# Optimization experiments

Hardware: AMD Instinct MI355X
Metric: run time of the kernel (lower is better)

## Reference

```python
import jax, jax.numpy as jnp
import numpy as np

DIM = 2048
HIDDEN = int(DIM * 2.6)  # 5324, matches int(dim*2.6) in torch
BATCH = 16384
EPS = 1e-12  # F.normalize default eps


def rmsnorm(x, g):
    # F.normalize(x, dim=-1) * dim**-0.5 * g
    n = jnp.linalg.norm(x, axis=-1, keepdims=True)
    return x / jnp.maximum(n, EPS) * (DIM ** -0.5) * g


def setup_inputs() -> dict:
    key = jax.random.key(0)
    ks = jax.random.split(key, 12)
    s = DIM ** -0.5
    return {
        "x": jax.random.normal(ks[0], (BATCH, DIM), jnp.float32),
        "state": jax.random.normal(ks[1], (BATCH, DIM), jnp.float32),
        "g1": jnp.ones((DIM,), jnp.float32),
        "g2": jnp.ones((DIM,), jnp.float32),
        "in_proj_w": jax.random.normal(ks[2], (3 * DIM, DIM), jnp.float32) * s,
        "in_proj_b": jnp.zeros((3 * DIM,), jnp.float32),
        "out_proj_w": jax.random.normal(ks[3], (DIM, DIM), jnp.float32) * s,
        "out_proj_b": jnp.zeros((DIM,), jnp.float32),
        "w1": jax.random.normal(ks[4], (HIDDEN, DIM), jnp.float32) * s,
        "w2": jax.random.normal(ks[5], (HIDDEN, DIM), jnp.float32) * s,
        "w3": jax.random.normal(ks[6], (DIM, HIDDEN), jnp.float32) * (HIDDEN ** -0.5),
    }


def reference(x, state, g1, g2, in_proj_w, in_proj_b, out_proj_w, out_proj_b, w1, w2, w3):
    h = x + state
    res = h
    hn = rmsnorm(h, g1)
    # MultiheadAttention with seq_len == 1: softmax over a single key is
    # exactly 1 for every head, so attn_out == out_proj(v_proj(hn)).
    wv = in_proj_w[2 * DIM:]
    bv = in_proj_b[2 * DIM:]
    v = hn @ wv.T + bv                      # [B, D]
    attn_out = v @ out_proj_w.T + out_proj_b
    h = res + attn_out
    hn2 = rmsnorm(h, g2)
    ffn = (jax.nn.silu(hn2 @ w1.T) * (hn2 @ w2.T)) @ w3.T
    return h + ffn
```

## Files before the change

### kernel.cpp

```cpp
#include <hip/hip_runtime.h>
#include <hip/hip_bf16.h>
#include <cstdint>
#include <cstddef>

#define DIMN   2048
#define BATCH  16384
#define HID    5324
#define HP     5376

typedef __bf16 bf16;
typedef __attribute__((ext_vector_type(8))) __bf16 bf16x8;
typedef __attribute__((ext_vector_type(4))) float floatx4;

#define GAS __attribute__((address_space(1)))
#define LAS __attribute__((address_space(3)))

__device__ __forceinline__ void async_copy16(const bf16* g, bf16* l) {
    __builtin_amdgcn_global_load_lds((const GAS uint32_t*)g, (LAS uint32_t*)l, 16, 0, 0);
}

template<int MODE>
__global__ __launch_bounds__(512, 2) void gemm_bt(
    const bf16* __restrict__ A, const bf16* __restrict__ W,
    const int K, const int N,
    const float* __restrict__ bias,
    float* __restrict__ f32io,
    bf16* __restrict__ bf16io)
{
    __shared__ __align__(16) bf16 lds[49152];

    const int tid  = threadIdx.x;
    const int lane = tid & 63;
    const int wv   = tid >> 6;
    const int wm   = wv >> 2;
    const int wn   = wv & 3;

    const int gx  = gridDim.x;
    const int nwg = gx * gridDim.y;
    int lin = blockIdx.y * gx + blockIdx.x;
    if ((nwg & 7) == 0) lin = (lin & 7) * (nwg >> 3) + (lin >> 3);
    const int bx = lin % gx, by = lin / gx;
    const int blockRow = by << 8;
    const int blockCol = bx << 8;

    const int sg = ((lane & 3) ^ ((lane >> 3) & 3)) * 8;
    const bf16* pA[2];
    const bf16* pB[2];
#pragma unroll
    for (int i = 0; i < 2; i++) {
        pA[i] = A + (size_t)(blockRow + i * 128 + wv * 16 + (lane >> 2)) * K + sg;
        pB[i] = W + (size_t)(blockCol + i * 128 + wv * 16 + (lane >> 2)) * K + sg;
    }

    const int m16 = lane & 15, quad = lane >> 4;
    const int rg = (quad ^ ((m16 >> 1) & 3)) * 8;
    const int aBase = (wm * 128 + m16) * 32 + rg;
    const int bBase = 8192 + (wn * 64 + m16) * 32 + rg;

    floatx4 acc[8][4];
    const floatx4 zero = {0.f, 0.f, 0.f, 0.f};
#pragma unroll
    for (int i = 0; i < 8; i++)
#pragma unroll
        for (int j = 0; j < 4; j++) acc[i][j] = zero;

    const int nt = K >> 5;

#pragma unroll
    for (int i = 0; i < 2; i++) {
        async_copy16(pA[i], &lds[i * 4096 + wv * 512]);
        async_copy16(pB[i], &lds[8192 + i * 4096 + wv * 512]);
    }
#pragma unroll
    for (int i = 0; i < 2; i++) { pA[i] += 32; pB[i] += 32; }
#pragma unroll
    for (int i = 0; i < 2; i++) {
        async_copy16(pA[i], &lds[16384 + i * 4096 + wv * 512]);
        async_copy16(pB[i], &lds[16384 + 8192 + i * 4096 + wv * 512]);
    }
#pragma unroll
    for (int i = 0; i < 2; i++) { pA[i] += 32; pB[i] += 32; }
    asm volatile("s_waitcnt vmcnt(4)" ::: "memory");
    __builtin_amdgcn_s_barrier();

    int sCur = 0, sNxt = 32768;
    for (int t = 0; t < nt; ++t) {
        const bool pf = (t + 2) < nt;

        if (pf) {
            async_copy16(pA[0], &lds[sNxt + wv * 512]);
            async_copy16(pA[1], &lds[sNxt + 4096 + wv * 512]);
        }
        bf16x8 bfr[4], afr[4];
#pragma unroll
        for (int j = 0; j < 4; j++) bfr[j] = *(const bf16x8*)&lds[sCur + bBase + j * 512];
#pragma unroll
        for (int i = 0; i < 4; i++) afr[i] = *(const bf16x8*)&lds[sCur + aBase + i * 512];
        __builtin_amdgcn_s_setprio(1);
#pragma unroll
        for (int i = 0; i < 4; i++)
#pragma unroll
            for (int j = 0; j < 4; j++)
                acc[i][j] = __builtin_amdgcn_mfma_f32_16x16x32_bf16(afr[i], bfr[j], acc[i][j], 0, 0, 0);
        __builtin_amdgcn_s_setprio(0);
        __builtin_amdgcn_s_barrier();

        if (pf) {
            async_copy16(pB[0], &lds[sNxt + 8192 + wv * 512]);
            async_copy16(pB[1], &lds[sNxt + 8192 + 4096 + wv * 512]);
            pA[0] += 32; pA[1] += 32; pB[0] += 32; pB[1] += 32;
        }
#pragma unroll
        for (int i = 0; i < 4; i++) afr[i] = *(const bf16x8*)&lds[sCur + aBase + 2048 + i * 512];
        __builtin_amdgcn_s_setprio(1);
#pragma unroll
        for (int i = 0; i < 4; i++)
#pragma unroll
            for (int j = 0; j < 4; j++)
                acc[i + 4][j] = __builtin_amdgcn_mfma_f32_16x16x32_bf16(afr[i], bfr[j], acc[i + 4][j], 0, 0, 0);
        __builtin_amdgcn_s_setprio(0);

        if (pf) { asm volatile("s_waitcnt vmcnt(4)" ::: "memory"); }
        else    { asm volatile("s_waitcnt vmcnt(0)" ::: "memory"); }
        __builtin_amdgcn_s_barrier();

        sCur = (sCur == 32768) ? 0 : sCur + 16384;
        sNxt = (sNxt == 32768) ? 0 : sNxt + 16384;
    }

#pragma unroll
    for (int j = 0; j < 4; j++) {
        const int col = blockCol + wn * 64 + j * 16 + m16;
        float bv = 0.f;
        if (MODE == 0 || MODE == 1) bv = bias[col];
#pragma unroll
        for (int i = 0; i < 8; i++) {
            const int row0 = blockRow + wm * 128 + i * 16 + quad * 4;
#pragma unroll
            for (int r = 0; r < 4; r++) {
                const size_t idx = (size_t)(row0 + r) * N + col;
                const float val = acc[i][j][r];
                if (MODE == 0) {
                    bf16io[idx] = (bf16)(val + bv);
                } else if (MODE == 1) {
                    f32io[idx] = f32io[idx] + val + bv;
                } else if (MODE == 2) {
                    bf16io[idx] = (bf16)(val / (1.f + __expf(-val)));
                } else if (MODE == 3) {
                    const float m = (float)bf16io[idx] * val;
                    bf16io[idx] = (bf16)m;
                } else {
                    f32io[idx] = f32io[idx] + val;
                }
            }
        }
    }
}

__global__ __launch_bounds__(256) void rms_add_kernel(
    const float* __restrict__ x, const float* __restrict__ st,
    const float* __restrict__ g, float* __restrict__ h, bf16* __restrict__ hn)
{
    const int row = blockIdx.x;
    const int tid = threadIdx.x;
    const float4* x4 = (const float4*)(x + (size_t)row * DIMN);
    const float4* s4 = (const float4*)(st + (size_t)row * DIMN);
    float4* h4 = (float4*)(h + (size_t)row * DIMN);
    const float4* g4 = (const float4*)g;

    float4 hv[2];
    float ss = 0.f;
#pragma unroll
    for (int c = 0; c < 2; c++) {
        const int i = tid + c * 256;
        const float4 a = x4[i];
        const float4 b = s4[i];
        float4 t;
        t.x = a.x + b.x; t.y = a.y + b.y; t.z = a.z + b.z; t.w = a.w + b.w;
        h4[i] = t;
        hv[c] = t;
        ss += t.x * t.x + t.y * t.y + t.z * t.z + t.w * t.w;
    }
#pragma unroll
    for (int off = 32; off; off >>= 1) ss += __shfl_xor(ss, off, 64);
    __shared__ float red[4];
    if ((tid & 63) == 0) red[tid >> 6] = ss;
    __syncthreads();
    const float tot = red[0] + red[1] + red[2] + red[3];
    const float scale = 0.02209708691207961f / fmaxf(sqrtf(tot), 1e-12f);

    bf16* o = hn + (size_t)row * DIMN;
#pragma unroll
    for (int c = 0; c < 2; c++) {
        const int i = tid + c * 256;
        const float4 gv = g4[i];
        const float4 t = hv[c];
        o[i * 4 + 0] = (bf16)(t.x * scale * gv.x);
        o[i * 4 + 1] = (bf16)(t.y * scale * gv.y);
        o[i * 4 + 2] = (bf16)(t.z * scale * gv.z);
        o[i * 4 + 3] = (bf16)(t.w * scale * gv.w);
    }
}

__global__ __launch_bounds__(256) void rms_kernel(
    const float* __restrict__ h, const float* __restrict__ g, bf16* __restrict__ hn)
{
    const int row = blockIdx.x;
    const int tid = threadIdx.x;
    const float4* h4 = (const float4*)(h + (size_t)row * DIMN);
    const float4* g4 = (const float4*)g;

    float4 hv[2];
    float ss = 0.f;
#pragma unroll
    for (int c = 0; c < 2; c++) {
        const int i = tid + c * 256;
        const float4 t = h4[i];
        hv[c] = t;
        ss += t.x * t.x + t.y * t.y + t.z * t.z + t.w * t.w;
    }
#pragma unroll
    for (int off = 32; off; off >>= 1) ss += __shfl_xor(ss, off, 64);
    __shared__ float red[4];
    if ((tid & 63) == 0) red[tid >> 6] = ss;
    __syncthreads();
    const float tot = red[0] + red[1] + red[2] + red[3];
    const float scale = 0.02209708691207961f / fmaxf(sqrtf(tot), 1e-12f);

    bf16* o = hn + (size_t)row * DIMN;
#pragma unroll
    for (int c = 0; c < 2; c++) {
        const int i = tid + c * 256;
        const float4 gv = g4[i];
        const float4 t = hv[c];
        o[i * 4 + 0] = (bf16)(t.x * scale * gv.x);
        o[i * 4 + 1] = (bf16)(t.y * scale * gv.y);
        o[i * 4 + 2] = (bf16)(t.z * scale * gv.z);
        o[i * 4 + 3] = (bf16)(t.w * scale * gv.w);
    }
}

__global__ __launch_bounds__(256) void cvt_pad_kernel(
    const float* __restrict__ src, bf16* __restrict__ dst,
    const int srcRows, const int srcCols, const int dstCols)
{
    const int col = blockIdx.x * 256 + threadIdx.x;
    const int row = blockIdx.y;
    if (col >= dstCols) return;
    float v = 0.f;
    if (row < srcRows && col < srcCols) v = src[(size_t)row * srcCols + col];
    dst[(size_t)row * dstCols + col] = (bf16)v;
}

extern "C" void kernel_launch(void* const* d_in, const int* in_sizes, int n_in,
                              void* d_out, int out_size, void* d_ws, size_t ws_size,
                              hipStream_t stream)
{
    const float* x   = (const float*)d_in[0];
    const float* st  = (const float*)d_in[1];
    const float* g1  = (const float*)d_in[2];
    const float* g2  = (const float*)d_in[3];
    const float* ipw = (const float*)d_in[4];
    const float* ipb = (const float*)d_in[5];
    const float* opw = (const float*)d_in[6];
    const float* opb = (const float*)d_in[7];
    const float* w1  = (const float*)d_in[8];
    const float* w2  = (const float*)d_in[9];
    const float* w3  = (const float*)d_in[10];
    float* out = (float*)d_out;

    char* wsb = (char*)d_ws;
    bf16* hn  = (bf16*)(wsb + 0);
    bf16* vb  = (bf16*)(wsb + 67108864);
    bf16* sa  = (bf16*)(wsb + 134217728);
    bf16* wvb = (bf16*)(wsb + 310378496);
    bf16* wob = (bf16*)(wsb + 318767104);
    bf16* w1b = (bf16*)(wsb + 327155712);
    bf16* w2b = (bf16*)(wsb + 349175808);
    bf16* w3b = (bf16*)(wsb + 371195904);

    cvt_pad_kernel<<<dim3(8, 2048), 256, 0, stream>>>(ipw + (size_t)2 * DIMN * DIMN, wvb, 2048, 2048, 2048);
    cvt_pad_kernel<<<dim3(8, 2048), 256, 0, stream>>>(opw, wob, 2048, 2048, 2048);
    cvt_pad_kernel<<<dim3(8, HP),   256, 0, stream>>>(w1, w1b, HID, 2048, 2048);
    cvt_pad_kernel<<<dim3(8, HP),   256, 0, stream>>>(w2, w2b, HID, 2048, 2048);
    cvt_pad_kernel<<<dim3(21, 2048),256, 0, stream>>>(w3, w3b, 2048, HID, HP);

    rms_add_kernel<<<BATCH, 256, 0, stream>>>(x, st, g1, out, hn);

    gemm_bt<0><<<dim3(8, 64), 512, 0, stream>>>(hn, wvb, 2048, 2048, ipb + 2 * DIMN, nullptr, vb);

    gemm_bt<1><<<dim3(8, 64), 512, 0, stream>>>(vb, wob, 2048, 2048, opb, out, nullptr);

    rms_kernel<<<BATCH, 256, 0, stream>>>(out, g2, hn);

    gemm_bt<2><<<dim3(21, 64), 512, 0, stream>>>(hn, w1b, 2048, HP, nullptr, nullptr, sa);

    gemm_bt<3><<<dim3(21, 64), 512, 0, stream>>>(hn, w2b, 2048, HP, nullptr, nullptr, sa);

    gemm_bt<4><<<dim3(8, 64), 512, 0, stream>>>(sa, w3b, HP, 2048, nullptr, out, nullptr);
}
```

Measured before the change: 2.210 ms.

## Split GEMM main loop into four barrier-separated MFMA phases interleaving loads

Restructures each K-iteration of the bf16 GEMM main loop into four quadrant phases (8 MFMAs each). Each phase issues a few LDS fragment reads and one async global-to-LDS copy, then places a sched_barrier and s_barrier before its MFMA block. The aim is to interleave memory traffic with matrix-core work across the waves sharing a CU, in a ping-pong style, and to spread the prefetch issue more evenly. In exchange it adds more workgroup barriers per iteration, which can cost synchronization overhead and may limit how freely the compiler can schedule instructions.

```diff
diff --git a/kernel.cpp b/kernel.cpp
--- a/kernel.cpp
+++ b/kernel.cpp
@@ -86,38 +86,61 @@
     int sCur = 0, sNxt = 32768;
     for (int t = 0; t < nt; ++t) {
         const bool pf = (t + 2) < nt;
+        bf16x8 a0[4], a1[4], b01[2], b23[2];
+
+#pragma unroll
+        for (int i = 0; i < 4; i++) a0[i] = *(const bf16x8*)&lds[sCur + aBase + i * 512];
+#pragma unroll
+        for (int j = 0; j < 2; j++) b01[j] = *(const bf16x8*)&lds[sCur + bBase + j * 512];
+        if (pf) async_copy16(pA[0], &lds[sNxt + wv * 512]);
+        __builtin_amdgcn_sched_barrier(0);
+        __builtin_amdgcn_s_barrier();
+        __builtin_amdgcn_s_setprio(1);
+#pragma unroll
+        for (int i = 0; i < 4; i++)
+#pragma unroll
+            for (int j = 0; j < 2; j++)
+                acc[i][j] = __builtin_amdgcn_mfma_f32_16x16x32_bf16(a0[i], b01[j], acc[i][j], 0, 0, 0);
+        __builtin_amdgcn_s_setprio(0);
+
+#pragma unroll
+        for (int i = 0; i < 4; i++) a1[i] = *(const bf16x8*)&lds[sCur + aBase + 2048 + i * 512];
+        if (pf) async_copy16(pA[1], &lds[sNxt + 4096 + wv * 512]);
+        __builtin_amdgcn_sched_barrier(0);
+        __builtin_amdgcn_s_barrier();
+        __builtin_amdgcn_s_setprio(1);
+#pragma unroll
+        for (int i = 0; i < 4; i++)
+#pragma unroll
+            for (int j = 0; j < 2; j++)
+                acc[i + 4][j] = __builtin_amdgcn_mfma_f32_16x16x32_bf16(a1[i], b01[j], acc[i + 4][j], 0, 0, 0);
+        __builtin_amdgcn_s_setprio(0);
+
+#pragma unroll
+        for (int j = 0; j < 2; j++) b23[j] = *(const bf16x8*)&lds[sCur + bBase + (2 + j) * 512];
+        if (pf) async_copy16(pB[0], &lds[sNxt + 8192 + wv * 512]);
+        __builtin_amdgcn_sched_barrier(0);
+        __builtin_amdgcn_s_barrier();
+        __builtin_amdgcn_s_setprio(1);
+#pragma unroll
+        for (int i = 0; i < 4; i++)
+#pragma unroll
+            for (int j = 0; j < 2; j++)
+                acc[i + 4][j + 2] = __builtin_amdgcn_mfma_f32_16x16x32_bf16(a1[i], b23[j], acc[i + 4][j + 2], 0, 0, 0);
+        __builtin_amdgcn_s_setprio(0);
 
         if (pf) {
-            async_copy16(pA[0], &lds[sNxt + wv * 512]);
-            async_copy16(pA[1], &lds[sNxt + 4096 + wv * 512]);
-        }
-        bf16x8 bfr[4], afr[4];
-#pragma unroll
-        for (int j = 0; j < 4; j++) bfr[j] = *(const bf16x8*)&lds[sCur + bBase + j * 512];
-#pragma unroll
-        for (int i = 0; i < 4; i++) afr[i] = *(const bf16x8*)&lds[sCur + aBase + i * 512];
-        __builtin_amdgcn_s_setprio(1);
-#pragma unroll
-        for (int i = 0; i < 4; i++)
-#pragma unroll
-            for (int j = 0; j < 4; j++)
-                acc[i][j] = __builtin_amdgcn_mfma_f32_16x16x32_bf16(afr[i], bfr[j], acc[i][j], 0, 0, 0);
-        __builtin_amdgcn_s_setprio(0);
-        __builtin_amdgcn_s_barrier();
-
-        if (pf) {
-            async_copy16(pB[0], &lds[sNxt + 8192 + wv * 512]);
             async_copy16(pB[1], &lds[sNxt + 8192 + 4096 + wv * 512]);
             pA[0] += 32; pA[1] += 32; pB[0] += 32; pB[1] += 32;
         }
-#pragma unroll
-        for (int i = 0; i < 4; i++) afr[i] = *(const bf16x8*)&lds[sCur + aBase + 2048 + i * 512];
+        __builtin_amdgcn_sched_barrier(0);
+        __builtin_amdgcn_s_barrier();
         __builtin_amdgcn_s_setprio(1);
 #pragma unroll
         for (int i = 0; i < 4; i++)
 #pragma unroll
-            for (int j = 0; j < 4; j++)
-                acc[i + 4][j] = __builtin_amdgcn_mfma_f32_16x16x32_bf16(afr[i], bfr[j], acc[i + 4][j], 0, 0, 0);
+            for (int j = 0; j < 2; j++)
+                acc[i][j + 2] = __builtin_amdgcn_mfma_f32_16x16x32_bf16(a0[i], b23[j], acc[i][j + 2], 0, 0, 0);
         __builtin_amdgcn_s_setprio(0);
 
         if (pf) { asm volatile("s_waitcnt vmcnt(4)" ::: "memory"); }
```

Measured after the change: 2.189 ms. Within noise of the previous version (-1.0%).
